# Kernel tuning notes

Hardware: AMD Instinct MI355X
Metric: run time of the kernel (lower is better)

Reference implementation:

```python
import jax, jax.numpy as jnp
import numpy as np

N, E, IN, H, OUT, L = 20000, 320000, 256, 256, 128, 3
EPS = 1e-5


def setup_inputs() -> dict:
    key = jax.random.key(0)
    ks = jax.random.split(key, 16)
    s = 0.02
    return {
        "x": jax.random.normal(ks[0], (N, IN), jnp.float32),
        "edge_index": jax.random.randint(ks[1], (2, E), 0, N, jnp.int64),
        "in_w": jax.random.normal(ks[2], (IN, H), jnp.float32) * s,
        "in_b": jnp.zeros((H,), jnp.float32),
        "parent_w": jax.random.normal(ks[3], (L, H, H), jnp.float32) * s,
        "child_w": jax.random.normal(ks[4], (L, H, H), jnp.float32) * s,
        "self_w": jax.random.normal(ks[5], (L, H, H), jnp.float32) * s,
        "self_b": jnp.zeros((L, H), jnp.float32),
        "ln_g": jnp.ones((L, H), jnp.float32),
        "ln_b": jnp.zeros((L, H), jnp.float32),
        "head_w1": jax.random.normal(ks[6], (H, H), jnp.float32) * s,
        "head_b1": jnp.zeros((H,), jnp.float32),
        "head_w2": jax.random.normal(ks[7], (H, OUT), jnp.float32) * s,
        "head_b2": jnp.zeros((OUT,), jnp.float32),
    }


def _aggregate(h, src, dst, weight):
    # gather -> matmul -> scatter-add -> degree-normalize
    transformed = h[src] @ weight                       # [E, H]
    agg = jax.ops.segment_sum(transformed, dst, num_segments=N)
    deg = jax.ops.segment_sum(jnp.ones((src.shape[0],), h.dtype), dst, num_segments=N)
    deg = jnp.maximum(deg, 1.0)
    return agg / deg[:, None]


def _layer_norm(x, g, b):
    mu = jnp.mean(x, axis=-1, keepdims=True)
    var = jnp.mean(jnp.square(x - mu), axis=-1, keepdims=True)
    return (x - mu) * jax.lax.rsqrt(var + EPS) * g + b


def reference(x, edge_index, in_w, in_b, parent_w, child_w, self_w, self_b,
              ln_g, ln_b, head_w1, head_b1, head_w2, head_b2):
    src, dst = edge_index[0], edge_index[1]
    h = x @ in_w + in_b                                  # input_proj
    for l in range(L):
        parent_msg = _aggregate(h, src, dst, parent_w[l])
        child_msg = _aggregate(h, dst, src, child_w[l])  # reversed edges
        out = h @ self_w[l] + self_b[l] + parent_msg + child_msg
        out = jax.nn.gelu(out, approximate=False)
        # dropout is identity in eval mode (training=False)
        h = _layer_norm(h + out, ln_g[l], ln_b[l])
    y = jax.nn.gelu(h @ head_w1 + head_b1, approximate=False)
    return y @ head_w2 + head_b2
```

## Files before the change

### kernel.cpp

```cpp
#include <hip/hip_runtime.h>


#define H 256
#define LAYERS 3
#define OUTD 128
#define LN_EPS 1e-5f

typedef short s16x8 __attribute__((ext_vector_type(8)));
typedef unsigned short u16x4 __attribute__((ext_vector_type(4)));
typedef unsigned short u16x8 __attribute__((ext_vector_type(8)));
typedef float f32x4 __attribute__((ext_vector_type(4)));
typedef int i32x4 __attribute__((ext_vector_type(4)));

__device__ __forceinline__ unsigned short f2bf(float f) {
  unsigned int u = __float_as_uint(f);
  u += 0x7FFFu + ((u >> 16) & 1u);
  return (unsigned short)(u >> 16);
}
__device__ __forceinline__ float bf2f(unsigned short s) {
  return __uint_as_float(((unsigned int)s) << 16);
}
__device__ __forceinline__ float gelu_f(float x) {
  return 0.5f * x * (1.0f + erff(x * 0.70710678118654752440f));
}
__device__ __forceinline__ void gload16(const void* g, void* l) {
  __builtin_amdgcn_global_load_lds((const __attribute__((address_space(1))) void*)g,
                                   (__attribute__((address_space(3))) void*)l, 16, 0, 0);
}


__device__ __forceinline__ void store_split8(unsigned short* __restrict__ T, int NS, int sec,
                                             int row, int l, u16x4 hv, u16x4 lv) {
  size_t tb = ((size_t)((row >> 4) * NS + sec) << 4) + (l >> 3);
  int off = (((row & 15) + (((l >> 1) & 3) << 4)) << 3) + ((l & 1) << 2);
  *(u16x4*)(T + tb * 512 + off) = hv;
  *(u16x4*)(T + (tb + 8) * 512 + off) = lv;
}

__global__ void split_tiles_kernel(const float* __restrict__ X,
                                   unsigned short* __restrict__ T, int NS,
                                   unsigned short* __restrict__ Hc, int M)
{
  const int rb = blockIdx.x;
  const int l = threadIdx.x & 63;
  const int cq = threadIdx.x >> 6;
  const int row = (rb << 4) + (l & 15);
  if (row >= M) return;
  const float* xr = X + (size_t)row * H;
#pragma unroll
  for (int p = 0; p < 2; ++p) {
    const int c = cq + (p << 2);
    const int j0 = (c << 5) + ((l >> 4) << 3);
    f32x4 v0 = *(const f32x4*)(xr + j0);
    f32x4 v1 = *(const f32x4*)(xr + j0 + 4);
    u16x8 hv, lv;
#pragma unroll
    for (int i = 0; i < 4; ++i) {
      unsigned short hb = f2bf(v0[i]); hv[i] = hb;     lv[i] = f2bf(v0[i] - bf2f(hb));
      unsigned short hc = f2bf(v1[i]); hv[4 + i] = hc; lv[4 + i] = f2bf(v1[i] - bf2f(hc));
    }
    size_t tb = ((size_t)(rb * NS) << 4);
    *(u16x8*)(T + (tb + c) * 512 + (l << 3)) = hv;
    *(u16x8*)(T + (tb + c + 8) * 512 + (l << 3)) = lv;
    if (Hc) *(u16x8*)(Hc + (size_t)row * H + j0) = hv;
  }
}

__global__ void bext_all_kernel(const float* __restrict__ in_w,
                                const float* __restrict__ parent_w,
                                const float* __restrict__ child_w,
                                const float* __restrict__ self_w,
                                const float* __restrict__ head_w1,
                                const float* __restrict__ head_w2,
                                unsigned short* __restrict__ Bext)
{
  const int slot = blockIdx.x >> 8;
  const int chunk = blockIdx.x & 255;
  const int ncol = (slot == 11) ? OUTD : H;
  const int idx = chunk * 256 + threadIdx.x;
  if (idx >= H * ncol) return;
  const float* W =
    (slot == 0)  ? in_w :
    (slot <= 3)  ? parent_w + (size_t)(slot - 1) * H * H :
    (slot <= 6)  ? child_w  + (size_t)(slot - 4) * H * H :
    (slot <= 9)  ? self_w   + (size_t)(slot - 7) * H * H :
    (slot == 10) ? head_w1  : head_w2;
  unsigned short* Bt = Bext + (size_t)slot * H * 512;
  int k = idx / ncol;
  int n = idx - k * ncol;
  float w = W[idx];
  unsigned short hb = f2bf(w);
  unsigned short lb = f2bf(w - bf2f(hb));
  size_t base = (((size_t)(n >> 4) << 4) + (k >> 5)) * 512 +
                (((n & 15) + (((k >> 3) & 3) << 4)) << 3) + (k & 7);
  Bt[base] = hb;
  Bt[base + 8 * 512] = lb;
}

__global__ void zero2_kernel(int* __restrict__ a, int* __restrict__ b, int n) {
  int i = blockIdx.x * 256 + threadIdx.x;
  if (i < n) { a[i] = 0; b[i] = 0; }
}

__global__ void deg_kernel(const int* __restrict__ src, const int* __restrict__ dst,
                           int* __restrict__ di, int* __restrict__ dox, int E) {
  int e = blockIdx.x * 256 + threadIdx.x;
  if (e >= E) return;
  atomicAdd(&dox[src[e]], 1);
  atomicAdd(&di[dst[e]], 1);
}

__global__ void rdeg_kernel(const int* __restrict__ di, const int* __restrict__ dox,
                            float* __restrict__ ri, float* __restrict__ ro,
                            int* __restrict__ cur_in, int* __restrict__ cur_out, int n) {
  int i = blockIdx.x * 256 + threadIdx.x;
  if (i >= n) return;
  int a = di[i];  if (a < 1) a = 1;
  int b = dox[i]; if (b < 1) b = 1;
  ri[i] = 1.0f / (float)a;
  ro[i] = 1.0f / (float)b;
  cur_in[i] = 0;
  cur_out[i] = 0;
}

__global__ __launch_bounds__(1024)
void scan2_kernel(const int* __restrict__ degi, const int* __restrict__ dego,
                  int* __restrict__ rp_in, int* __restrict__ rp_out, int n) {
  __shared__ int partial[1024];
  const int* deg = blockIdx.x ? dego : degi;
  int* rowptr = blockIdx.x ? rp_out : rp_in;
  const int t = threadIdx.x;
  const int chunk = (n + 1023) / 1024;
  int b = t * chunk;
  int e = b + chunk; if (e > n) e = n;
  int s = 0;
  for (int i = b; i < e; ++i) s += deg[i];
  partial[t] = s;
  __syncthreads();
  for (int off = 1; off < 1024; off <<= 1) {
    int v = (t >= off) ? partial[t - off] : 0;
    __syncthreads();
    partial[t] += v;
    __syncthreads();
  }
  int run = (t == 0) ? 0 : partial[t - 1];
  for (int i = b; i < e; ++i) { rowptr[i] = run; run += deg[i]; }
  if (t == 1023) rowptr[n] = run;
}

__global__ void fill_kernel(const int* __restrict__ src, const int* __restrict__ dst,
                            const int* __restrict__ rp_in, const int* __restrict__ rp_out,
                            int* __restrict__ cur_in, int* __restrict__ cur_out,
                            int* __restrict__ ci_in, int* __restrict__ ci_out, int E) {
  int e = blockIdx.x * 256 + threadIdx.x;
  if (e >= E) return;
  int s = src[e], d = dst[e];
  int p = atomicAdd(&cur_in[d], 1);
  ci_in[rp_in[d] + p] = s;
  int q = atomicAdd(&cur_out[s], 1);
  ci_out[rp_out[s] + q] = d;
}

template<int NF, int GELU, int SPLIT>
__global__ __launch_bounds__(256)
void gemm_kernel(const unsigned short* __restrict__ A, int NSa,
                 const unsigned short* __restrict__ B0,
                 const unsigned short* __restrict__ B1,
                 const unsigned short* __restrict__ B2,
                 const float* __restrict__ bias, float* __restrict__ C,
                 unsigned short* __restrict__ Asp, int NSp,
                 unsigned short* __restrict__ Hc,
                 int M, int nrb, int nsec)
{
  constexpr int N = NF * 64;
  __shared__ unsigned short ldsA[2][2048];

  const int tid = threadIdx.x;
  const int lane = tid & 63;
  const int wn = tid >> 6;
  const int m0 = blockIdx.x << 5;
  int rbw = (blockIdx.x << 1) + (wn & 1);
  if (rbw >= nrb) rbw = nrb - 1;
  const int hilo = wn >> 1;

  f32x4 acc[2][NF] = {};

  auto STAGE = [&](int buf, int step) {
    const int s = step >> 3;
    const int c = step & 7;
    const unsigned short* pa =
        A + (((size_t)(rbw * NSa + s) << 4) + c + (hilo << 3)) * 512 + (lane << 3);
    gload16(pa, &ldsA[buf][0] + (wn << 9));
  };

  auto COMPUTE = [&](int buf, int step) {
    const int s = step >> 3;
    const int c = step & 7;
    const unsigned short* Bs = (s == 0) ? B0 : ((s == 1) ? B1 : B2);
    s16x8 bh[NF], bl[NF];
#pragma unroll
    for (int j = 0; j < NF; ++j) {
      const int g = wn * NF + j;
      bh[j] = *(const s16x8*)(Bs + ((size_t)((g << 4) + c) << 9) + (lane << 3));
      bl[j] = *(const s16x8*)(Bs + ((size_t)((g << 4) + c + 8) << 9) + (lane << 3));
    }
    const unsigned short* base = &ldsA[buf][0];
    s16x8 ah[2], al[2];
#pragma unroll
    for (int f = 0; f < 2; ++f) {
      ah[f] = *(const s16x8*)(base + (f << 9) + (lane << 3));
      al[f] = *(const s16x8*)(base + 1024 + (f << 9) + (lane << 3));
    }
#pragma unroll
    for (int i = 0; i < 2; ++i)
#pragma unroll
      for (int j = 0; j < NF; ++j)
        acc[i][j] = __builtin_amdgcn_mfma_f32_16x16x32_bf16(ah[i], bh[j], acc[i][j], 0, 0, 0);
#pragma unroll
    for (int i = 0; i < 2; ++i)
#pragma unroll
      for (int j = 0; j < NF; ++j)
        acc[i][j] = __builtin_amdgcn_mfma_f32_16x16x32_bf16(ah[i], bl[j], acc[i][j], 0, 0, 0);
#pragma unroll
    for (int i = 0; i < 2; ++i)
#pragma unroll
      for (int j = 0; j < NF; ++j)
        acc[i][j] = __builtin_amdgcn_mfma_f32_16x16x32_bf16(al[i], bh[j], acc[i][j], 0, 0, 0);
  };

  const int nsteps = nsec << 3;
  STAGE(0, 0);
  int cur = 0;
  for (int t = 0; t < nsteps - 1; ++t) {
    STAGE(cur ^ 1, t + 1);
    asm volatile("s_waitcnt vmcnt(1)" ::: "memory");
    __builtin_amdgcn_s_barrier();
    COMPUTE(cur, t);
    asm volatile("s_waitcnt lgkmcnt(0)" ::: "memory");
    __builtin_amdgcn_s_barrier();
    cur ^= 1;
  }
  asm volatile("s_waitcnt vmcnt(0)" ::: "memory");
  __builtin_amdgcn_s_barrier();
  COMPUTE(cur, nsteps - 1);

  const int r0 = (lane >> 4) << 2;
  const int cn = lane & 15;
#pragma unroll
  for (int j = 0; j < NF; ++j) {
    const int col = wn * (NF << 4) + (j << 4) + cn;
    const float bb = bias ? bias[col] : 0.0f;
#pragma unroll
    for (int i = 0; i < 2; ++i) {
      const int rowb = m0 + (i << 4) + r0;
#pragma unroll
      for (int r = 0; r < 4; ++r) {
        const int rr = rowb + r;
        if (rr < M) {
          float v = acc[i][j][r] + bb;
          if (GELU) v = gelu_f(v);
          if (C) C[(size_t)rr * N + col] = v;
          if (SPLIT) {
            unsigned short hb = f2bf(v);
            size_t tb = (((size_t)(rr >> 4) * NSp) << 4) + (col >> 5);
            int off = ((rr & 15) << 3) + (((col >> 3) & 3) << 7) + (col & 7);
            Asp[tb * 512 + off] = hb;
            Asp[(tb + 8) * 512 + off] = f2bf(v - bf2f(hb));
            if (Hc) Hc[((size_t)rr << 8) + col] = hb;
          }
        }
      }
    }
  }
}

__device__ __forceinline__ void gacc8(const int* __restrict__ ci, int beg, int end,
                                      const unsigned short* __restrict__ Hc, int foff,
                                      float* __restrict__ acc) {
  int i = beg;
  for (; i < end && (i & 3); ++i) {
    u16x8 a = *(const u16x8*)(Hc + ((size_t)ci[i] << 8) + foff);
#pragma unroll
    for (int z = 0; z < 8; ++z) acc[z] += bf2f(a[z]);
  }
  for (; i + 8 <= end; i += 8) {
    i32x4 id0 = *(const i32x4*)(ci + i);
    i32x4 id1 = *(const i32x4*)(ci + i + 4);
    u16x8 a0 = *(const u16x8*)(Hc + ((size_t)id0[0] << 8) + foff);
    u16x8 a1 = *(const u16x8*)(Hc + ((size_t)id0[1] << 8) + foff);
    u16x8 a2 = *(const u16x8*)(Hc + ((size_t)id0[2] << 8) + foff);
    u16x8 a3 = *(const u16x8*)(Hc + ((size_t)id0[3] << 8) + foff);
    u16x8 a4 = *(const u16x8*)(Hc + ((size_t)id1[0] << 8) + foff);
    u16x8 a5 = *(const u16x8*)(Hc + ((size_t)id1[1] << 8) + foff);
    u16x8 a6 = *(const u16x8*)(Hc + ((size_t)id1[2] << 8) + foff);
    u16x8 a7 = *(const u16x8*)(Hc + ((size_t)id1[3] << 8) + foff);
#pragma unroll
    for (int z = 0; z < 8; ++z)
      acc[z] += ((bf2f(a0[z]) + bf2f(a1[z])) + (bf2f(a2[z]) + bf2f(a3[z]))) +
                ((bf2f(a4[z]) + bf2f(a5[z])) + (bf2f(a6[z]) + bf2f(a7[z])));
  }
  for (; i + 4 <= end; i += 4) {
    i32x4 id = *(const i32x4*)(ci + i);
    u16x8 a = *(const u16x8*)(Hc + ((size_t)id[0] << 8) + foff);
    u16x8 b = *(const u16x8*)(Hc + ((size_t)id[1] << 8) + foff);
    u16x8 c = *(const u16x8*)(Hc + ((size_t)id[2] << 8) + foff);
    u16x8 d = *(const u16x8*)(Hc + ((size_t)id[3] << 8) + foff);
#pragma unroll
    for (int z = 0; z < 8; ++z)
      acc[z] += (bf2f(a[z]) + bf2f(b[z])) + (bf2f(c[z]) + bf2f(d[z]));
  }
  for (; i < end; ++i) {
    u16x8 a = *(const u16x8*)(Hc + ((size_t)ci[i] << 8) + foff);
#pragma unroll
    for (int z = 0; z < 8; ++z) acc[z] += bf2f(a[z]);
  }
}

__global__ __launch_bounds__(256)
void gather_kernel(
    const int* __restrict__ rp_in, const int* __restrict__ ci_in,
    const int* __restrict__ rp_out, const int* __restrict__ ci_out,
    const float* __restrict__ ri, const float* __restrict__ ro,
    const unsigned short* __restrict__ Hc, unsigned short* __restrict__ Aext,
    int M, int nrb)
{
  __shared__ unsigned short sh[2][2][2][512];
  const int b = blockIdx.x;
  const int xcd = b & 7;
  const int s = xcd >> 1;
  const int rb = ((b >> 3) << 1) + (xcd & 1);
  if (rb >= nrb) return;
  const int tid = threadIdx.x;
  const int d = tid >> 7;
  const int g = (tid >> 3) & 15;
  const int t = tid & 7;
  const int row = (rb << 4) + g;
  const int foff = (s << 6) + (t << 3);

  float acc[8] = {};
  float wsc = 0.f;
  if (row < M) {
    const int* __restrict__ ci = d ? ci_out : ci_in;
    const int* __restrict__ rp = d ? rp_out : rp_in;
    gacc8(ci, rp[row], rp[row + 1], Hc, foff, acc);
    wsc = d ? ro[row] : ri[row];
  }

  const int cc = t >> 2;
  const int pos = (g << 3) + ((t & 3) << 7);
  u16x8 hv, lv;
#pragma unroll
  for (int q = 0; q < 8; ++q) {
    float v = acc[q] * wsc;
    unsigned short hb = f2bf(v);
    hv[q] = hb; lv[q] = f2bf(v - bf2f(hb));
  }
  *(u16x8*)(&sh[d][0][cc][pos]) = hv;
  *(u16x8*)(&sh[d][1][cc][pos]) = lv;
  __syncthreads();

  const int tp = tid >> 5;
  const int q = tid & 31;
  const int sec = tp >> 2, hilo = (tp >> 1) & 1, c2 = tp & 1;
  const int cg = (s << 1) + c2 + (hilo << 3);
  size_t tile = ((size_t)(rb * 3 + 1 + sec) << 4) + cg;
  unsigned short* dstp = Aext + tile * 512;
  const unsigned short* srcp = &sh[sec][hilo][c2][0];
#pragma unroll
  for (int i = 0; i < 2; ++i)
    *(u16x8*)(dstp + (i << 8) + (q << 3)) = *(const u16x8*)(srcp + (i << 8) + (q << 3));
}

__global__ void finalize_kernel(float* __restrict__ h, const float* __restrict__ P,
                                unsigned short* __restrict__ Aext,
                                unsigned short* __restrict__ Hc,
                                const float* __restrict__ g, const float* __restrict__ b, int M)
{
  int row = blockIdx.x * 4 + (threadIdx.x >> 6);
  if (row >= M) return;
  int l = threadIdx.x & 63;
  int j = l << 2;
  f32x4 hv = *(const f32x4*)(h + (size_t)row * H + j);
  f32x4 pv = *(const f32x4*)(P + (size_t)row * H + j);
  f32x4 t;
  float sum = 0.f, sq = 0.f;
#pragma unroll
  for (int i = 0; i < 4; ++i) {
    t[i] = hv[i] + gelu_f(pv[i]);
    sum += t[i];
    sq += t[i] * t[i];
  }
#pragma unroll
  for (int off = 1; off < 64; off <<= 1) {
    sum += __shfl_xor(sum, off, 64);
    sq  += __shfl_xor(sq, off, 64);
  }
  float mu = sum * (1.0f / H);
  float var = sq * (1.0f / H) - mu * mu;
  float rs = rsqrtf(var + LN_EPS);
  f32x4 outv;
  u16x4 hvv, lvv;
#pragma unroll
  for (int i = 0; i < 4; ++i) {
    outv[i] = (t[i] - mu) * rs * g[j + i] + b[j + i];
    unsigned short hb = f2bf(outv[i]);
    hvv[i] = hb;
    lvv[i] = f2bf(outv[i] - bf2f(hb));
  }
  *(f32x4*)(h + (size_t)row * H + j) = outv;
  *(u16x4*)(Hc + ((size_t)row << 8) + j) = hvv;
  store_split8(Aext, 3, 0, row, l, hvv, lvv);
}

extern "C" void kernel_launch(void* const* d_in, const int* in_sizes, int n_in,
                              void* d_out, int out_size, void* d_ws, size_t ws_size,
                              hipStream_t stream)
{
  const float* x        = (const float*)d_in[0];
  const int*   ei       = (const int*)d_in[1];
  const float* in_w     = (const float*)d_in[2];
  const float* in_b     = (const float*)d_in[3];
  const float* parent_w = (const float*)d_in[4];
  const float* child_w  = (const float*)d_in[5];
  const float* self_w   = (const float*)d_in[6];
  const float* self_b   = (const float*)d_in[7];
  const float* ln_g     = (const float*)d_in[8];
  const float* ln_b     = (const float*)d_in[9];
  const float* head_w1  = (const float*)d_in[10];
  const float* head_b1  = (const float*)d_in[11];
  const float* head_w2  = (const float*)d_in[12];
  const float* head_b2  = (const float*)d_in[13];

  const int M = in_sizes[0] / H;
  const int E = in_sizes[1] / 2;
  const int nrb = (M + 15) / 16;
  const int* src = ei;
  const int* dst = ei + E;

  char* w = (char*)d_ws;
  auto alloc = [&](size_t bytes) { char* p = w; w += (bytes + 255) & ~(size_t)255; return p; };
  float*          h    = (float*)alloc((size_t)M * H * 4);
  float*          P    = (float*)alloc((size_t)M * H * 4);
  unsigned short* Ax   = (unsigned short*)alloc((size_t)nrb * 16 * 512 * 2);
  unsigned short* Aext = (unsigned short*)alloc((size_t)nrb * 48 * 512 * 2);
  unsigned short* Hc   = (unsigned short*)alloc((size_t)M * H * 2);
  unsigned short* Bext = (unsigned short*)alloc((size_t)12 * H * 512 * 2);
  int*            degi = (int*)alloc((size_t)M * 4);
  int*            dego = (int*)alloc((size_t)M * 4);
  float*          ri   = (float*)alloc((size_t)M * 4);
  float*          ro   = (float*)alloc((size_t)M * 4);
  int*            rp_in   = (int*)alloc((size_t)(M + 1) * 4);
  int*            rp_out  = (int*)alloc((size_t)(M + 1) * 4);
  int*            cur_in  = (int*)alloc((size_t)M * 4);
  int*            cur_out = (int*)alloc((size_t)M * 4);
  int*            ci_in   = (int*)alloc((size_t)E * 4);
  int*            ci_out  = (int*)alloc((size_t)E * 4);
  if ((size_t)(w - (char*)d_ws) > ws_size) return;

  auto bslot = [&](int i) { return Bext + (size_t)i * H * 512; };

  bext_all_kernel<<<12 * 256, 256, 0, stream>>>(in_w, parent_w, child_w, self_w,
                                                head_w1, head_w2, Bext);

  zero2_kernel<<<(M + 255) / 256, 256, 0, stream>>>(degi, dego, M);
  deg_kernel<<<(E + 255) / 256, 256, 0, stream>>>(src, dst, degi, dego, E);
  rdeg_kernel<<<(M + 255) / 256, 256, 0, stream>>>(degi, dego, ri, ro, cur_in, cur_out, M);
  scan2_kernel<<<2, 1024, 0, stream>>>(degi, dego, rp_in, rp_out, M);
  fill_kernel<<<(E + 255) / 256, 256, 0, stream>>>(src, dst, rp_in, rp_out,
                                                   cur_in, cur_out, ci_in, ci_out, E);

  const int mb32 = (M + 31) / 32;
  const int ggrid = (M + 3) / 4;
  const int xgrid = 8 * ((nrb + 1) / 2);

  split_tiles_kernel<<<nrb, 256, 0, stream>>>(x, Ax, 1, nullptr, M);
  gemm_kernel<4, 0, 1><<<mb32, 256, 0, stream>>>(Ax, 1, bslot(0), nullptr, nullptr,
                                                 in_b, h, Aext, 3, Hc, M, nrb, 1);

  for (int l = 0; l < LAYERS; ++l) {
    gather_kernel<<<xgrid, 256, 0, stream>>>(rp_in, ci_in, rp_out, ci_out,
                                             ri, ro, Hc, Aext, M, nrb);
    gemm_kernel<4, 0, 0><<<mb32, 256, 0, stream>>>(Aext, 3,
                                                   bslot(7 + l), bslot(1 + l), bslot(4 + l),
                                                   self_b + (size_t)l * H, P,
                                                   nullptr, 0, nullptr, M, nrb, 3);
    finalize_kernel<<<ggrid, 256, 0, stream>>>(h, P, Aext, Hc,
                                               ln_g + (size_t)l * H, ln_b + (size_t)l * H, M);
  }

  gemm_kernel<4, 1, 1><<<mb32, 256, 0, stream>>>(Aext, 3, bslot(10), nullptr, nullptr,
                                                 head_b1, nullptr, Ax, 1, nullptr, M, nrb, 1);
  gemm_kernel<2, 0, 0><<<mb32, 256, 0, stream>>>(Ax, 1, bslot(11), nullptr, nullptr,
                                                 head_b2, (float*)d_out, nullptr, 0, nullptr,
                                                 M, nrb, 1);
}
```

Before: 442.0 us.

## Overlap self-weight GEMM with neighbor gather in a fused per-layer kernel

Each layer's GEMM is split in two. The self-projection part (h @ self_w + bias) now runs inside the same launch as the edge gather, in blocks with a higher block index. A second GEMM then adds the parent and child aggregation products on top of P by reading the existing output back. This lets the compute-bound self GEMM overlap the memory-bound gather instead of waiting for it, at the cost of an extra read-modify-write pass over P and one more launch per layer.

```diff
diff --git a/kernel.cpp b/kernel.cpp
--- a/kernel.cpp
+++ b/kernel.cpp
@@ -161,25 +161,21 @@
   ci_out[rp_out[s] + q] = d;
 }
 
-template<int NF, int GELU, int SPLIT>
-__global__ __launch_bounds__(256)
-void gemm_kernel(const unsigned short* __restrict__ A, int NSa,
-                 const unsigned short* __restrict__ B0,
-                 const unsigned short* __restrict__ B1,
-                 const unsigned short* __restrict__ B2,
-                 const float* __restrict__ bias, float* __restrict__ C,
-                 unsigned short* __restrict__ Asp, int NSp,
-                 unsigned short* __restrict__ Hc,
-                 int M, int nrb, int nsec)
+template<int NF, int GELU, int SPLIT, int ACCUM>
+__device__ __forceinline__ void gemm_body(
+    unsigned short* __restrict__ ldsA, int bid,
+    const unsigned short* __restrict__ A, int NSa,
+    const unsigned short* __restrict__ B0, const unsigned short* __restrict__ B1,
+    const float* __restrict__ bias, float* __restrict__ C,
+    unsigned short* __restrict__ Asp, int NSp, unsigned short* __restrict__ Hc,
+    int M, int nrb, int nsec)
 {
   constexpr int N = NF * 64;
-  __shared__ unsigned short ldsA[2][2048];
-
   const int tid = threadIdx.x;
   const int lane = tid & 63;
   const int wn = tid >> 6;
-  const int m0 = blockIdx.x << 5;
-  int rbw = (blockIdx.x << 1) + (wn & 1);
+  const int m0 = bid << 5;
+  int rbw = (bid << 1) + (wn & 1);
   if (rbw >= nrb) rbw = nrb - 1;
   const int hilo = wn >> 1;
 
@@ -190,13 +186,13 @@
     const int c = step & 7;
     const unsigned short* pa =
         A + (((size_t)(rbw * NSa + s) << 4) + c + (hilo << 3)) * 512 + (lane << 3);
-    gload16(pa, &ldsA[buf][0] + (wn << 9));
+    gload16(pa, ldsA + (buf << 11) + (wn << 9));
   };
 
   auto COMPUTE = [&](int buf, int step) {
     const int s = step >> 3;
     const int c = step & 7;
-    const unsigned short* Bs = (s == 0) ? B0 : ((s == 1) ? B1 : B2);
+    const unsigned short* Bs = (s == 0) ? B0 : B1;
     s16x8 bh[NF], bl[NF];
 #pragma unroll
     for (int j = 0; j < NF; ++j) {
@@ -204,7 +200,7 @@
       bh[j] = *(const s16x8*)(Bs + ((size_t)((g << 4) + c) << 9) + (lane << 3));
       bl[j] = *(const s16x8*)(Bs + ((size_t)((g << 4) + c + 8) << 9) + (lane << 3));
     }
-    const unsigned short* base = &ldsA[buf][0];
+    const unsigned short* base = ldsA + (buf << 11);
     s16x8 ah[2], al[2];
 #pragma unroll
     for (int f = 0; f < 2; ++f) {
@@ -258,6 +254,7 @@
         const int rr = rowb + r;
         if (rr < M) {
           float v = acc[i][j][r] + bb;
+          if (ACCUM) v += C[(size_t)rr * N + col];
           if (GELU) v = gelu_f(v);
           if (C) C[(size_t)rr * N + col] = v;
           if (SPLIT) {
@@ -274,6 +271,21 @@
   }
 }
 
+template<int NF, int GELU, int SPLIT, int ACCUM>
+__global__ __launch_bounds__(256)
+void gemm_kernel(const unsigned short* __restrict__ A, int NSa,
+                 const unsigned short* __restrict__ B0,
+                 const unsigned short* __restrict__ B1,
+                 const float* __restrict__ bias, float* __restrict__ C,
+                 unsigned short* __restrict__ Asp, int NSp,
+                 unsigned short* __restrict__ Hc,
+                 int M, int nrb, int nsec)
+{
+  __shared__ unsigned short ldsA[2 * 2048];
+  gemm_body<NF, GELU, SPLIT, ACCUM>(ldsA, blockIdx.x, A, NSa, B0, B1,
+                                    bias, C, Asp, NSp, Hc, M, nrb, nsec);
+}
+
 __device__ __forceinline__ void gacc8(const int* __restrict__ ci, int beg, int end,
                                       const unsigned short* __restrict__ Hc, int foff,
                                       float* __restrict__ acc) {
@@ -316,16 +328,14 @@
   }
 }
 
-__global__ __launch_bounds__(256)
-void gather_kernel(
+__device__ __forceinline__ void gather_body(
+    unsigned short* __restrict__ sh, int b,
     const int* __restrict__ rp_in, const int* __restrict__ ci_in,
     const int* __restrict__ rp_out, const int* __restrict__ ci_out,
     const float* __restrict__ ri, const float* __restrict__ ro,
     const unsigned short* __restrict__ Hc, unsigned short* __restrict__ Aext,
     int M, int nrb)
 {
-  __shared__ unsigned short sh[2][2][2][512];
-  const int b = blockIdx.x;
   const int xcd = b & 7;
   const int s = xcd >> 1;
   const int rb = ((b >> 3) << 1) + (xcd & 1);
@@ -355,8 +365,8 @@
     unsigned short hb = f2bf(v);
     hv[q] = hb; lv[q] = f2bf(v - bf2f(hb));
   }
-  *(u16x8*)(&sh[d][0][cc][pos]) = hv;
-  *(u16x8*)(&sh[d][1][cc][pos]) = lv;
+  *(u16x8*)(sh + (((d << 1) + 0) << 10) + (cc << 9) + pos) = hv;
+  *(u16x8*)(sh + (((d << 1) + 1) << 10) + (cc << 9) + pos) = lv;
   __syncthreads();
 
   const int tp = tid >> 5;
@@ -365,10 +375,29 @@
   const int cg = (s << 1) + c2 + (hilo << 3);
   size_t tile = ((size_t)(rb * 3 + 1 + sec) << 4) + cg;
   unsigned short* dstp = Aext + tile * 512;
-  const unsigned short* srcp = &sh[sec][hilo][c2][0];
+  const unsigned short* srcp = sh + (((sec << 1) + hilo) << 10) + (c2 << 9);
 #pragma unroll
   for (int i = 0; i < 2; ++i)
     *(u16x8*)(dstp + (i << 8) + (q << 3)) = *(const u16x8*)(srcp + (i << 8) + (q << 3));
+}
+
+__global__ __launch_bounds__(256)
+void layer_fused_kernel(
+    const int* __restrict__ rp_in, const int* __restrict__ ci_in,
+    const int* __restrict__ rp_out, const int* __restrict__ ci_out,
+    const float* __restrict__ ri, const float* __restrict__ ro,
+    const unsigned short* __restrict__ Hc, unsigned short* __restrict__ Aext,
+    const unsigned short* __restrict__ Bself, const float* __restrict__ self_b,
+    float* __restrict__ P, int M, int nrb, int ngather)
+{
+  __shared__ unsigned short smem[4096];
+  const int b = blockIdx.x;
+  if (b < ngather) {
+    gather_body(smem, b, rp_in, ci_in, rp_out, ci_out, ri, ro, Hc, Aext, M, nrb);
+  } else {
+    gemm_body<4, 0, 0, 0>(smem, b - ngather, Aext, 3, Bself, Bself,
+                          self_b, P, nullptr, 0, nullptr, M, nrb, 1);
+  }
 }
 
 __global__ void finalize_kernel(float* __restrict__ h, const float* __restrict__ P,
@@ -474,23 +503,23 @@
   const int xgrid = 8 * ((nrb + 1) / 2);
 
   split_tiles_kernel<<<nrb, 256, 0, stream>>>(x, Ax, 1, nullptr, M);
-  gemm_kernel<4, 0, 1><<<mb32, 256, 0, stream>>>(Ax, 1, bslot(0), nullptr, nullptr,
-                                                 in_b, h, Aext, 3, Hc, M, nrb, 1);
+  gemm_kernel<4, 0, 1, 0><<<mb32, 256, 0, stream>>>(Ax, 1, bslot(0), bslot(0),
+                                                    in_b, h, Aext, 3, Hc, M, nrb, 1);
 
   for (int l = 0; l < LAYERS; ++l) {
-    gather_kernel<<<xgrid, 256, 0, stream>>>(rp_in, ci_in, rp_out, ci_out,
-                                             ri, ro, Hc, Aext, M, nrb);
-    gemm_kernel<4, 0, 0><<<mb32, 256, 0, stream>>>(Aext, 3,
-                                                   bslot(7 + l), bslot(1 + l), bslot(4 + l),
-                                                   self_b + (size_t)l * H, P,
-                                                   nullptr, 0, nullptr, M, nrb, 3);
+    layer_fused_kernel<<<xgrid + mb32, 256, 0, stream>>>(
+        rp_in, ci_in, rp_out, ci_out, ri, ro, Hc, Aext,
+        bslot(7 + l), self_b + (size_t)l * H, P, M, nrb, xgrid);
+    gemm_kernel<4, 0, 0, 1><<<mb32, 256, 0, stream>>>(
+        Aext + 16 * 512, 3, bslot(1 + l), bslot(4 + l),
+        nullptr, P, nullptr, 0, nullptr, M, nrb, 2);
     finalize_kernel<<<ggrid, 256, 0, stream>>>(h, P, Aext, Hc,
                                                ln_g + (size_t)l * H, ln_b + (size_t)l * H, M);
   }
 
-  gemm_kernel<4, 1, 1><<<mb32, 256, 0, stream>>>(Aext, 3, bslot(10), nullptr, nullptr,
-                                                 head_b1, nullptr, Ax, 1, nullptr, M, nrb, 1);
-  gemm_kernel<2, 0, 0><<<mb32, 256, 0, stream>>>(Ax, 1, bslot(11), nullptr, nullptr,
-                                                 head_b2, (float*)d_out, nullptr, 0, nullptr,
-                                                 M, nrb, 1);
-}
+  gemm_kernel<4, 1, 1, 0><<<mb32, 256, 0, stream>>>(Aext, 3, bslot(10), bslot(10),
+                                                    head_b1, nullptr, Ax, 1, nullptr, M, nrb, 1);
+  gemm_kernel<2, 0, 0, 0><<<mb32, 256, 0, stream>>>(Ax, 1, bslot(11), bslot(11),
+                                                    head_b2, (float*)d_out, nullptr, 0, nullptr,
+                                                    M, nrb, 1);
+}
```

Result: slower. 507.3 us (+14.8%).
